# Performance work log

Hardware: AMD Instinct MI355X
Metric: run time of the kernel (lower is better)

## Reference

```python
import jax, jax.numpy as jnp
import numpy as np

N_ATOMS = 1_000_000
N_GRAPHS = 8192
FEA_DIM = 64
HIDDEN = 32
N_HEAD = 3


def setup_inputs() -> dict:
    key = jax.random.key(0)
    k1, k2, k3, k4, k5, k6 = jax.random.split(key, 6)
    atom_feas = jax.random.normal(k1, (N_ATOMS, FEA_DIM), dtype=jnp.float32)
    atom_owner = jnp.sort(jax.random.randint(k2, (N_ATOMS,), 0, N_GRAPHS))
    s1 = 1.0 / np.sqrt(FEA_DIM)
    s2 = 1.0 / np.sqrt(HIDDEN)
    W1 = jax.random.uniform(k3, (FEA_DIM, HIDDEN), jnp.float32, -s1, s1)
    b1 = jax.random.uniform(k4, (HIDDEN,), jnp.float32, -s1, s1)
    W2 = jax.random.uniform(k5, (HIDDEN, N_HEAD), jnp.float32, -s2, s2)
    b2 = jax.random.uniform(k6, (N_HEAD,), jnp.float32, -s2, s2)
    return {"atom_feas": atom_feas, "atom_owner": atom_owner,
            "W1": W1, "b1": b1, "W2": W2, "b2": b2}


def reference(atom_feas, atom_owner, W1, b1, W2, b2):
    # key MLP: Linear -> SiLU -> Linear, producing per-atom, per-head logits [N, H]
    h = jax.nn.silu(atom_feas @ W1 + b1)
    logits = h @ W2 + b2  # [N, H]
    # per-graph (segment) softmax over atoms, independently per head
    seg_max = jax.ops.segment_max(logits, atom_owner, num_segments=N_GRAPHS)  # [G, H]
    e = jnp.exp(logits - seg_max[atom_owner])
    denom = jax.ops.segment_sum(e, atom_owner, num_segments=N_GRAPHS)  # [G, H]
    w = e / denom[atom_owner]  # [N, H]
    # attention-weighted pooling: per graph, atom_fea.T @ w -> [D, H] flattened row-major
    outer = (atom_feas[:, :, None] * w[:, None, :]).reshape(atom_feas.shape[0], FEA_DIM * N_HEAD)
    crystal_feas = jax.ops.segment_sum(outer, atom_owner, num_segments=N_GRAPHS)  # [G, D*H]
    return crystal_feas
```

## Files before the change

### kernel.cpp

```cpp
#include <hip/hip_runtime.h>
#include <math.h>
#include <stdint.h>

#define NFEA  64
#define NHEAD 3
#define GPB   2
#define CH    64

typedef float v2f __attribute__((ext_vector_type(2)));

__device__ __forceinline__ void wave_sync_lds() {
  asm volatile("s_waitcnt lgkmcnt(0)" ::: "memory");
}
__device__ __forceinline__ void wait_vm0() {
  asm volatile("s_waitcnt vmcnt(0)" ::: "memory");
}

__global__ void gar_starts(const int* __restrict__ owner, int* __restrict__ starts,
                           int n_atoms, int n_graphs)
{
  int a = blockIdx.x * blockDim.x + threadIdx.x;
  if (a >= n_atoms) return;
  int cur  = owner[a];
  int prev = (a == 0) ? -1 : owner[a - 1];
  for (int g = prev + 1; g <= cur; ++g) starts[g] = a;
  if (a == n_atoms - 1)
    for (int g = cur + 1; g <= n_graphs; ++g) starts[g] = n_atoms;
}

__global__ __launch_bounds__(GPB * 64, 4) void gar_main(
    const float* __restrict__ atom_feas,
    const int*   __restrict__ starts,
    const float* __restrict__ W1, const float* __restrict__ b1,
    const float* __restrict__ W2, const float* __restrict__ b2,
    float* __restrict__ out, int n_graphs, int n_atoms)
{
  __shared__ __align__(16) float xl_all[GPB][CH * NFEA];
  const int w = threadIdx.x >> 6;
  const int t = threadIdx.x & 63;
  const int g = blockIdx.x * GPB + w;
  if (g >= n_graphs) return;
  float* xl = xl_all[w];

  const int s0 = starts[g];
  const int n  = starts[g + 1] - s0;
  float* __restrict__ outg = out + (size_t)g * (NFEA * NHEAD);
  if (n <= 0) {
    outg[t * 3 + 0] = 0.f; outg[t * 3 + 1] = 0.f; outg[t * 3 + 2] = 0.f;
    return;
  }

  unsigned offp[4];
#pragma unroll
  for (int jm = 0; jm < 4; ++jm) {
    int i = jm * 4 + (t >> 4);
    int s = (t & 15) ^ (i & 15);
    offp[jm] = (unsigned)(i * 256 + s * 16);
  }
  const unsigned max_src = (unsigned)n_atoms * 256u - 16u;
  const char* __restrict__ xbytes = (const char*)atom_feas;

  float m0 = -INFINITY, m1 = -INFINITY, m2 = -INFINITY;
  float d0 = 0.f, d1 = 0.f, d2 = 0.f;
  float a0 = 0.f, a1 = 0.f, a2 = 0.f;

  const int nc = (n + CH - 1) / CH;
  const int isw = (t & 15);
  const int prow = (t >> 2) << 2;
  const int pcol = (t & 3);

  for (int c = 0; c < nc; ++c) {
    wave_sync_lds();
    const unsigned cbase = (unsigned)(s0 + c * CH) * 256u;
#pragma unroll
    for (int j = 0; j < 16; ++j) {
      unsigned src = cbase + offp[j & 3] + (unsigned)((j >> 2) * 4096);
      if (src > max_src) src = max_src;
      __builtin_amdgcn_global_load_lds(
          (const __attribute__((address_space(1))) void*)(xbytes + src),
          (__attribute__((address_space(3))) void*)(xl + j * 256),
          16, 0, 0);
    }
    wait_vm0();

    v2f h[16];
#pragma unroll
    for (int j = 0; j < 16; ++j) h[j] = ((const v2f*)b1)[j];
    const int ibase = t * 64;
#pragma unroll
    for (int q = 0; q < 16; ++q) {
      float4 xq = *(const float4*)(xl + ibase + ((q ^ isw) << 2));
      float xs[4] = {xq.x, xq.y, xq.z, xq.w};
#pragma unroll
      for (int dd = 0; dd < 4; ++dd) {
        v2f xd2 = {xs[dd], xs[dd]};
        const v2f* wrow = ((const v2f*)W1) + (q * 4 + dd) * 16;
#pragma unroll
        for (int jj = 0; jj < 16; ++jj)
          h[jj] = __builtin_elementwise_fma(xd2, wrow[jj], h[jj]);
      }
    }
    float l0 = b2[0], l1 = b2[1], l2 = b2[2];
#pragma unroll
    for (int jj = 0; jj < 16; ++jj) {
#pragma unroll
      for (int cc = 0; cc < 2; ++cc) {
        float hj = h[jj][cc];
        float s = hj * __builtin_amdgcn_rcpf(1.0f + __expf(-hj));
        int k = 2 * jj + cc;
        l0 = fmaf(s, W2[k * 3 + 0], l0);
        l1 = fmaf(s, W2[k * 3 + 1], l1);
        l2 = fmaf(s, W2[k * 3 + 2], l2);
      }
    }
    const bool act = (c * CH + t) < n;
    if (!act) { l0 = -INFINITY; l1 = -INFINITY; l2 = -INFINITY; }

    float c0 = l0, c1 = l1, c2 = l2;
#pragma unroll
    for (int off = 32; off > 0; off >>= 1) {
      c0 = fmaxf(c0, __shfl_xor(c0, off));
      c1 = fmaxf(c1, __shfl_xor(c1, off));
      c2 = fmaxf(c2, __shfl_xor(c2, off));
    }
    const float n0 = fmaxf(m0, c0), n1 = fmaxf(m1, c1), n2 = fmaxf(m2, c2);
    const float r0 = __expf(m0 - n0), r1 = __expf(m1 - n1), r2 = __expf(m2 - n2);
    m0 = n0; m1 = n1; m2 = n2;

    const float e0 = __expf(l0 - n0);
    const float e1 = __expf(l1 - n1);
    const float e2 = __expf(l2 - n2);
    float s0s = e0, s1s = e1, s2s = e2;
#pragma unroll
    for (int off = 32; off > 0; off >>= 1) {
      s0s += __shfl_xor(s0s, off);
      s1s += __shfl_xor(s1s, off);
      s2s += __shfl_xor(s2s, off);
    }
    d0 = d0 * r0 + s0s;
    d1 = d1 * r1 + s1s;
    d2 = d2 * r2 + s2s;

    a0 *= r0; a1 *= r1; a2 *= r2;
    int cnt = n - c * CH; if (cnt > CH) cnt = CH;
#pragma unroll 4
    for (int a = 0; a < cnt; ++a) {
      float xv = xl[a * 64 + (prow ^ ((a & 15) << 2)) + pcol];
      float ea0 = __shfl(e0, a);
      float ea1 = __shfl(e1, a);
      float ea2 = __shfl(e2, a);
      a0 = fmaf(ea0, xv, a0);
      a1 = fmaf(ea1, xv, a1);
      a2 = fmaf(ea2, xv, a2);
    }
  }

  const float i0 = 1.f / d0, i1 = 1.f / d1, i2 = 1.f / d2;
  outg[t * 3 + 0] = a0 * i0;
  outg[t * 3 + 1] = a1 * i1;
  outg[t * 3 + 2] = a2 * i2;
}

extern "C" void kernel_launch(void* const* d_in, const int* in_sizes, int n_in,
                              void* d_out, int out_size, void* d_ws, size_t ws_size,
                              hipStream_t stream)
{
  const float* atom_feas = (const float*)d_in[0];
  const int*   owner     = (const int*)d_in[1];
  const float* W1        = (const float*)d_in[2];
  const float* b1        = (const float*)d_in[3];
  const float* W2        = (const float*)d_in[4];
  const float* b2        = (const float*)d_in[5];
  float* out = (float*)d_out;

  const int n_atoms  = in_sizes[1];
  const int n_graphs = out_size / (NFEA * NHEAD);

  int* starts = (int*)d_ws;

  hipLaunchKernelGGL(gar_starts, dim3((n_atoms + 255) / 256), dim3(256), 0, stream,
                     owner, starts, n_atoms, n_graphs);
  hipLaunchKernelGGL(gar_main, dim3((n_graphs + GPB - 1) / GPB), dim3(GPB * 64), 0, stream,
                     atom_feas, starts, W1, b1, W2, b2, out, n_graphs, n_atoms);
}
```

Before: 465.4 us.

## Split fused segment-attention kernel into persistent MLP pass and pooling pass

Replaces the single per-graph kernel, which ran the MLP and an online softmax on 64-atom chunks, with two kernels. The first is a persistent, double-buffered MLP kernel over fixed 256-atom tiles that writes per-atom logits to workspace. The second is a per-graph pooling kernel that reads the logits, computes max and sum directly, caches exp values in LDS and accumulates the weighted features straight from global memory. This removes per-graph load imbalance and the online-softmax rescaling in the MLP phase, at the cost of reading atom_feas twice plus an extra logits round trip and a third launch.

```diff
diff --git a/kernel.cpp b/kernel.cpp
--- a/kernel.cpp
+++ b/kernel.cpp
@@ -2,18 +2,17 @@
 #include <math.h>
 #include <stdint.h>
 
-#define NFEA  64
-#define NHEAD 3
-#define GPB   2
-#define CH    64
+#define NFEA   64
+#define NHEAD  3
+#define K1_T   256
+#define K1_TILE 256
+#define GPB    4
+#define LCAP   256
 
 typedef float v2f __attribute__((ext_vector_type(2)));
 
 __device__ __forceinline__ void wave_sync_lds() {
   asm volatile("s_waitcnt lgkmcnt(0)" ::: "memory");
-}
-__device__ __forceinline__ void wait_vm0() {
-  asm volatile("s_waitcnt vmcnt(0)" ::: "memory");
 }
 
 __global__ void gar_starts(const int* __restrict__ owner, int* __restrict__ starts,
@@ -28,72 +27,62 @@
     for (int g = cur + 1; g <= n_graphs; ++g) starts[g] = n_atoms;
 }
 
-__global__ __launch_bounds__(GPB * 64, 4) void gar_main(
+__global__ __launch_bounds__(K1_T, 1) void gar_mlp(
     const float* __restrict__ atom_feas,
-    const int*   __restrict__ starts,
     const float* __restrict__ W1, const float* __restrict__ b1,
     const float* __restrict__ W2, const float* __restrict__ b2,
-    float* __restrict__ out, int n_graphs, int n_atoms)
-{
-  __shared__ __align__(16) float xl_all[GPB][CH * NFEA];
-  const int w = threadIdx.x >> 6;
-  const int t = threadIdx.x & 63;
-  const int g = blockIdx.x * GPB + w;
-  if (g >= n_graphs) return;
-  float* xl = xl_all[w];
-
-  const int s0 = starts[g];
-  const int n  = starts[g + 1] - s0;
-  float* __restrict__ outg = out + (size_t)g * (NFEA * NHEAD);
-  if (n <= 0) {
-    outg[t * 3 + 0] = 0.f; outg[t * 3 + 1] = 0.f; outg[t * 3 + 2] = 0.f;
-    return;
-  }
-
-  unsigned offp[4];
-#pragma unroll
-  for (int jm = 0; jm < 4; ++jm) {
-    int i = jm * 4 + (t >> 4);
-    int s = (t & 15) ^ (i & 15);
-    offp[jm] = (unsigned)(i * 256 + s * 16);
-  }
-  const unsigned max_src = (unsigned)n_atoms * 256u - 16u;
+    float4* __restrict__ logits4, int n_atoms, int n_tiles)
+{
+  __shared__ __align__(16) float xs[2][K1_TILE * NFEA];
+  const int tid = threadIdx.x;
+  const int w = tid >> 6, t = tid & 63;
   const char* __restrict__ xbytes = (const char*)atom_feas;
 
-  float m0 = -INFINITY, m1 = -INFINITY, m2 = -INFINITY;
-  float d0 = 0.f, d1 = 0.f, d2 = 0.f;
-  float a0 = 0.f, a1 = 0.f, a2 = 0.f;
-
-  const int nc = (n + CH - 1) / CH;
-  const int isw = (t & 15);
-  const int prow = (t >> 2) << 2;
-  const int pcol = (t & 3);
-
-  for (int c = 0; c < nc; ++c) {
-    wave_sync_lds();
-    const unsigned cbase = (unsigned)(s0 + c * CH) * 256u;
+  auto STAGE = [&](int tile, int buf) {
+    const unsigned base_row = (unsigned)tile * K1_TILE;
 #pragma unroll
     for (int j = 0; j < 16; ++j) {
-      unsigned src = cbase + offp[j & 3] + (unsigned)((j >> 2) * 4096);
-      if (src > max_src) src = max_src;
+      const int r = ((j * 4 + w) << 2) + (t >> 4);
+      unsigned grow = base_row + (unsigned)r;
+      if (grow >= (unsigned)n_atoms) grow = (unsigned)n_atoms - 1;
+      const unsigned src = grow * 256u + (unsigned)((((t & 15) ^ (r & 15)) << 4));
       __builtin_amdgcn_global_load_lds(
           (const __attribute__((address_space(1))) void*)(xbytes + src),
-          (__attribute__((address_space(3))) void*)(xl + j * 256),
+          (__attribute__((address_space(3))) void*)
+              ((char*)&xs[buf][0] + ((j * 4 + w) << 10) + (t << 4)),
           16, 0, 0);
     }
-    wait_vm0();
-
+  };
+
+  int tile = blockIdx.x;
+  if (tile >= n_tiles) return;
+  STAGE(tile, 0);
+  int buf = 0;
+  const int key = (tid & 15);
+
+  for (; tile < n_tiles; tile += gridDim.x) {
+    const int nxt = tile + gridDim.x;
+    if (nxt < n_tiles) {
+      STAGE(nxt, buf ^ 1);
+      asm volatile("s_waitcnt vmcnt(16)" ::: "memory");
+    } else {
+      asm volatile("s_waitcnt vmcnt(0)" ::: "memory");
+    }
+    asm volatile("" ::: "memory");
+    __builtin_amdgcn_s_barrier();
+    asm volatile("" ::: "memory");
+
+    const float* xrow = &xs[buf][tid * 64];
     v2f h[16];
 #pragma unroll
     for (int j = 0; j < 16; ++j) h[j] = ((const v2f*)b1)[j];
-    const int ibase = t * 64;
 #pragma unroll
     for (int q = 0; q < 16; ++q) {
-      float4 xq = *(const float4*)(xl + ibase + ((q ^ isw) << 2));
-      float xs[4] = {xq.x, xq.y, xq.z, xq.w};
+      float4 xq = *(const float4*)(xrow + ((q ^ key) << 2));
+      float xsc[4] = {xq.x, xq.y, xq.z, xq.w};
 #pragma unroll
       for (int dd = 0; dd < 4; ++dd) {
-        v2f xd2 = {xs[dd], xs[dd]};
+        v2f xd2 = {xsc[dd], xsc[dd]};
         const v2f* wrow = ((const v2f*)W1) + (q * 4 + dd) * 16;
 #pragma unroll
         for (int jj = 0; jj < 16; ++jj)
@@ -113,46 +102,101 @@
         l2 = fmaf(s, W2[k * 3 + 2], l2);
       }
     }
-    const bool act = (c * CH + t) < n;
-    if (!act) { l0 = -INFINITY; l1 = -INFINITY; l2 = -INFINITY; }
-
-    float c0 = l0, c1 = l1, c2 = l2;
-#pragma unroll
-    for (int off = 32; off > 0; off >>= 1) {
-      c0 = fmaxf(c0, __shfl_xor(c0, off));
-      c1 = fmaxf(c1, __shfl_xor(c1, off));
-      c2 = fmaxf(c2, __shfl_xor(c2, off));
-    }
-    const float n0 = fmaxf(m0, c0), n1 = fmaxf(m1, c1), n2 = fmaxf(m2, c2);
-    const float r0 = __expf(m0 - n0), r1 = __expf(m1 - n1), r2 = __expf(m2 - n2);
-    m0 = n0; m1 = n1; m2 = n2;
-
-    const float e0 = __expf(l0 - n0);
-    const float e1 = __expf(l1 - n1);
-    const float e2 = __expf(l2 - n2);
-    float s0s = e0, s1s = e1, s2s = e2;
-#pragma unroll
-    for (int off = 32; off > 0; off >>= 1) {
-      s0s += __shfl_xor(s0s, off);
-      s1s += __shfl_xor(s1s, off);
-      s2s += __shfl_xor(s2s, off);
-    }
-    d0 = d0 * r0 + s0s;
-    d1 = d1 * r1 + s1s;
-    d2 = d2 * r2 + s2s;
-
-    a0 *= r0; a1 *= r1; a2 *= r2;
-    int cnt = n - c * CH; if (cnt > CH) cnt = CH;
+    const int aabs = tile * K1_TILE + tid;
+    if (aabs < n_atoms) logits4[aabs] = make_float4(l0, l1, l2, 0.f);
+
+    asm volatile("" ::: "memory");
+    __builtin_amdgcn_s_barrier();
+    asm volatile("" ::: "memory");
+    buf ^= 1;
+  }
+}
+
+__global__ __launch_bounds__(GPB * 64, 8) void gar_pool(
+    const float* __restrict__ atom_feas,
+    const int*   __restrict__ starts,
+    const float4* __restrict__ logits4,
+    float* __restrict__ out, int n_graphs)
+{
+  __shared__ __align__(16) float4 e4[GPB][LCAP];
+  const int w = threadIdx.x >> 6, t = threadIdx.x & 63;
+  const int g = blockIdx.x * GPB + w;
+  if (g >= n_graphs) return;
+  const int s0 = starts[g];
+  const int n  = starts[g + 1] - s0;
+  float* __restrict__ outg = out + (size_t)g * (NFEA * NHEAD);
+  if (n <= 0) {
+    outg[t * 3 + 0] = 0.f; outg[t * 3 + 1] = 0.f; outg[t * 3 + 2] = 0.f;
+    return;
+  }
+
+  float lr[4][3];
+  float m0 = -INFINITY, m1 = -INFINITY, m2 = -INFINITY;
+#pragma unroll
+  for (int c = 0; c < 4; ++c) {
+    if (c * 64 < n) {
+      int i = c * 64 + t;
+      bool act = i < n;
+      float4 lv = logits4[s0 + (act ? i : 0)];
+      lr[c][0] = act ? lv.x : -INFINITY;
+      lr[c][1] = act ? lv.y : -INFINITY;
+      lr[c][2] = act ? lv.z : -INFINITY;
+      m0 = fmaxf(m0, lr[c][0]); m1 = fmaxf(m1, lr[c][1]); m2 = fmaxf(m2, lr[c][2]);
+    } else {
+      lr[c][0] = -INFINITY; lr[c][1] = -INFINITY; lr[c][2] = -INFINITY;
+    }
+  }
+  for (int i = 4 * 64 + t; i < n; i += 64) {
+    float4 lv = logits4[s0 + i];
+    m0 = fmaxf(m0, lv.x); m1 = fmaxf(m1, lv.y); m2 = fmaxf(m2, lv.z);
+  }
+#pragma unroll
+  for (int off = 32; off > 0; off >>= 1) {
+    m0 = fmaxf(m0, __shfl_xor(m0, off));
+    m1 = fmaxf(m1, __shfl_xor(m1, off));
+    m2 = fmaxf(m2, __shfl_xor(m2, off));
+  }
+
+  float d0 = 0.f, d1 = 0.f, d2 = 0.f;
+#pragma unroll
+  for (int c = 0; c < 4; ++c) {
+    if (c * 64 < n) {
+      float e0 = __expf(lr[c][0] - m0);
+      float e1 = __expf(lr[c][1] - m1);
+      float e2 = __expf(lr[c][2] - m2);
+      d0 += e0; d1 += e1; d2 += e2;
+      e4[w][c * 64 + t] = make_float4(e0, e1, e2, 0.f);
+    }
+  }
+  for (int i = 4 * 64 + t; i < n; i += 64) {
+    float4 lv = logits4[s0 + i];
+    d0 += __expf(lv.x - m0); d1 += __expf(lv.y - m1); d2 += __expf(lv.z - m2);
+  }
+#pragma unroll
+  for (int off = 32; off > 0; off >>= 1) {
+    d0 += __shfl_xor(d0, off);
+    d1 += __shfl_xor(d1, off);
+    d2 += __shfl_xor(d2, off);
+  }
+  wave_sync_lds();
+
+  float a0 = 0.f, a1 = 0.f, a2 = 0.f;
+  const float* __restrict__ xcol = atom_feas + (size_t)s0 * NFEA + t;
+  const int nmain = n < LCAP ? n : LCAP;
 #pragma unroll 4
-    for (int a = 0; a < cnt; ++a) {
-      float xv = xl[a * 64 + (prow ^ ((a & 15) << 2)) + pcol];
-      float ea0 = __shfl(e0, a);
-      float ea1 = __shfl(e1, a);
-      float ea2 = __shfl(e2, a);
-      a0 = fmaf(ea0, xv, a0);
-      a1 = fmaf(ea1, xv, a1);
-      a2 = fmaf(ea2, xv, a2);
-    }
+  for (int a = 0; a < nmain; ++a) {
+    float  xv = xcol[(size_t)a * NFEA];
+    float4 ev = e4[w][a];
+    a0 = fmaf(ev.x, xv, a0);
+    a1 = fmaf(ev.y, xv, a1);
+    a2 = fmaf(ev.z, xv, a2);
+  }
+  for (int a = LCAP; a < n; ++a) {
+    float4 lv = logits4[s0 + a];
+    float  xv = xcol[(size_t)a * NFEA];
+    a0 = fmaf(__expf(lv.x - m0), xv, a0);
+    a1 = fmaf(__expf(lv.y - m1), xv, a1);
+    a2 = fmaf(__expf(lv.z - m2), xv, a2);
   }
 
   const float i0 = 1.f / d0, i1 = 1.f / d1, i2 = 1.f / d2;
@@ -177,9 +221,16 @@
   const int n_graphs = out_size / (NFEA * NHEAD);
 
   int* starts = (int*)d_ws;
+  const size_t log_off = (((size_t)(n_graphs + 1) * sizeof(int)) + 255) & ~(size_t)255;
+  float4* logits4 = (float4*)((char*)d_ws + log_off);
+
+  const int n_tiles = (n_atoms + K1_TILE - 1) / K1_TILE;
+  const int k1_grid = n_tiles < 256 ? n_tiles : 256;
 
   hipLaunchKernelGGL(gar_starts, dim3((n_atoms + 255) / 256), dim3(256), 0, stream,
                      owner, starts, n_atoms, n_graphs);
-  hipLaunchKernelGGL(gar_main, dim3((n_graphs + GPB - 1) / GPB), dim3(GPB * 64), 0, stream,
-                     atom_feas, starts, W1, b1, W2, b2, out, n_graphs, n_atoms);
-}
+  hipLaunchKernelGGL(gar_mlp, dim3(k1_grid), dim3(K1_T), 0, stream,
+                     atom_feas, W1, b1, W2, b2, logits4, n_atoms, n_tiles);
+  hipLaunchKernelGGL(gar_pool, dim3((n_graphs + GPB - 1) / GPB), dim3(GPB * 64), 0, stream,
+                     atom_feas, starts, logits4, out, n_graphs);
+}
```

Result: slower. 501.1 us (+7.7%).
